# Optimization experiments

Measured on AMD Instinct MI355X. Metric: run time of the kernel, lower is better.

The kernel has to match this reference:

```python
import jax, jax.numpy as jnp
import numpy as np

D_MODEL = 1024
NUM_HEADS = 16
D_HEAD = D_MODEL // NUM_HEADS
ROPE_THETA = 10000.0


def _rope(x, pos):
    # x: [..., S, d_head]; rotate consecutive pairs (2i, 2i+1)
    half = x.shape[-1] // 2
    inv_freq = ROPE_THETA ** (-jnp.arange(half, dtype=jnp.float32) * 2.0 / x.shape[-1])
    ang = pos[:, None].astype(jnp.float32) * inv_freq[None, :]  # [S, half]
    cos, sin = jnp.cos(ang), jnp.sin(ang)
    x1, x2 = x[..., 0::2], x[..., 1::2]
    r1 = x1 * cos - x2 * sin
    r2 = x1 * sin + x2 * cos
    return jnp.stack([r1, r2], axis=-1).reshape(x.shape)


def setup_inputs() -> dict:
    key = jax.random.key(0)
    ks = jax.random.split(key, 5)
    s = 1.0 / np.sqrt(D_MODEL)
    return {
        "q_weight": jax.random.normal(ks[0], (D_MODEL, D_MODEL), jnp.float32) * s,
        "k_weight": jax.random.normal(ks[1], (D_MODEL, D_MODEL), jnp.float32) * s,
        "v_weight": jax.random.normal(ks[2], (D_MODEL, D_MODEL), jnp.float32) * s,
        "o_weight": jax.random.normal(ks[3], (D_MODEL, D_MODEL), jnp.float32) * s,
        "in_features": jax.random.normal(ks[4], (2, 2048, D_MODEL), jnp.float32),
    }


def reference(q_weight, k_weight, v_weight, o_weight, in_features):
    S = in_features.shape[-2]
    qw = q_weight.reshape(NUM_HEADS, D_HEAD, D_MODEL)
    kw = k_weight.reshape(NUM_HEADS, D_HEAD, D_MODEL)
    vw = v_weight.reshape(NUM_HEADS, D_HEAD, D_MODEL)
    # [B, H, S, d_head]
    q = jnp.einsum('bsj,nhj->bnsh', in_features, qw)
    k = jnp.einsum('bsj,nhj->bnsh', in_features, kw)
    v = jnp.einsum('bsj,nhj->bnsh', in_features, vw)
    pos = jnp.arange(S)
    q = _rope(q, pos)
    k = _rope(k, pos)
    scale = 1.0 / jnp.sqrt(jnp.asarray(D_HEAD, dtype=q.dtype))
    scores = jnp.einsum('bnqh,bnkh->bnqk', q, k) * scale  # [B,H,S,S]
    causal = jnp.tril(jnp.ones((S, S), dtype=bool))
    scores = jnp.where(causal, scores, jnp.asarray(-jnp.inf, dtype=scores.dtype))
    attn = jax.nn.softmax(scores, axis=-1)
    out = jnp.einsum('bnqk,bnkh->bnqh', attn, v)  # [B,H,S,d_head]
    out = jnp.swapaxes(out, -2, -3).reshape(*out.shape[:-3], S, D_MODEL)
    return jnp.einsum('ji,bki->bkj', o_weight, out)
```

## Files before the change

kernel.cpp:

```cpp
#include <hip/hip_runtime.h>
#include <math.h>

typedef __attribute__((ext_vector_type(8))) short bf16x8;
typedef __attribute__((ext_vector_type(4))) float f32x4;
typedef __attribute__((ext_vector_type(2))) unsigned int u32x2;

static constexpr int D_MODEL = 1024;
static constexpr int SEQ = 2048;
static constexpr int BATCH = 2;
static constexpr int M_TOT = BATCH * SEQ;

__device__ __forceinline__ unsigned short f2bf(float f) {
  unsigned int u = __builtin_bit_cast(unsigned int, f);
  u += 0x7fffu + ((u >> 16) & 1u);
  return (unsigned short)(u >> 16);
}

__device__ __forceinline__ unsigned int cvtpk(float lo, float hi) {
  unsigned int r;
  asm volatile("v_cvt_pk_bf16_f32 %0, %1, %2" : "=v"(r) : "v"(lo), "v"(hi));
  return r;
}

__device__ __forceinline__ void gld16(const unsigned short* g, unsigned short* l) {
  __builtin_amdgcn_global_load_lds(
      (const __attribute__((address_space(1))) unsigned int*)g,
      (__attribute__((address_space(3))) unsigned int*)l, 16, 0, 0);
}

__global__ void cvt_f32_bf16(const float* __restrict__ src,
                             unsigned short* __restrict__ dst, int n4) {
  int i = blockIdx.x * blockDim.x + threadIdx.x;
  if (i >= n4) return;
  const float4 v = reinterpret_cast<const float4*>(src)[i];
  ushort4 o;
  o.x = f2bf(v.x); o.y = f2bf(v.y); o.z = f2bf(v.z); o.w = f2bf(v.w);
  reinterpret_cast<ushort4*>(dst)[i] = o;
}

__global__ void cvt_weights(const float* __restrict__ qw, const float* __restrict__ kw,
                            const float* __restrict__ vw, const float* __restrict__ ow,
                            unsigned short* __restrict__ dst) {
  int i = blockIdx.x * blockDim.x + threadIdx.x;
  const int which = i >> 18;
  const int off = i & 262143;
  const float* src = (which == 0) ? qw : (which == 1) ? kw : (which == 2) ? vw : ow;
  const float4 v = reinterpret_cast<const float4*>(src)[off];
  ushort4 o;
  o.x = f2bf(v.x); o.y = f2bf(v.y); o.z = f2bf(v.z); o.w = f2bf(v.w);
  reinterpret_cast<ushort4*>(dst)[i] = o;
}

__global__ void rope_tables(float2* __restrict__ ct2) {
  int idx = blockIdx.x * blockDim.x + threadIdx.x;
  int s = idx >> 5;
  int p = idx & 31;
  float inv_freq = powf(10000.0f, -(float)p / 32.0f);
  float ang = (float)s * inv_freq;
  int psw = p ^ (((s >> 2) & 1) << 3);
  float2 cs; cs.x = cosf(ang); cs.y = sinf(ang);
  ct2[s * 32 + psw] = cs;
}

template <int BM, int BN, int MODE>
__global__ __launch_bounds__(256, 2)
void gemm2(const unsigned short* __restrict__ A,
           const unsigned short* __restrict__ W,
           unsigned short* __restrict__ Qd,
           unsigned short* __restrict__ Kd,
           unsigned short* __restrict__ Vd,
           float* __restrict__ Fd,
           const float2* __restrict__ ct2) {
  constexpr int MI = BM / 32, NI = BN / 32;
  constexpr int NKT = D_MODEL / 32;
  constexpr int LOADS = BM / 64 + BN / 64;
  __shared__ __align__(16) unsigned short smem[2 * (BM + BN) * 32];
  unsigned short* Asm = smem;
  unsigned short* Bsm = smem + 2 * BM * 32;
  const int tid  = threadIdx.x;
  const int lane = tid & 63;
  const int wave = tid >> 6;
  const int wm = wave >> 1, wn = wave & 1;
  const int m0 = blockIdx.y * BM;
  const int n0 = blockIdx.x * BN;
  const int lr = lane & 15, lg = lane >> 4;

  const int srow = lane >> 2;
  const int scol = ((lane & 3) ^ ((lane >> 3) & 3)) * 8;

  auto stage = [&](int buf, int kt) {
    const int k0 = kt * 32;
#pragma unroll
    for (int rr = 0; rr < BM / 64; ++rr) {
      const int ch = rr * 4 + wave;
      gld16(&A[(size_t)(m0 + ch * 16 + srow) * D_MODEL + k0 + scol], &Asm[buf * BM * 32 + ch * 512]);
    }
#pragma unroll
    for (int rr = 0; rr < BN / 64; ++rr) {
      const int ch = rr * 4 + wave;
      gld16(&W[(size_t)(n0 + ch * 16 + srow) * D_MODEL + k0 + scol], &Bsm[buf * BN * 32 + ch * 512]);
    }
  };

  f32x4 acc[MI][NI] = {};

  stage(0, 0);
  stage(1, 1);
  __builtin_amdgcn_sched_barrier(0);

  const int swz = (lg ^ ((lr >> 1) & 3)) * 8;

  for (int kt = 0; kt < NKT; ++kt) {
    const int cur = kt & 1;
    if (kt + 1 < NKT) {
      if constexpr (LOADS == 4) asm volatile("s_waitcnt vmcnt(4)" ::: "memory");
      else                      asm volatile("s_waitcnt vmcnt(3)" ::: "memory");
    } else {
      asm volatile("s_waitcnt vmcnt(0)" ::: "memory");
    }
    __builtin_amdgcn_s_barrier();
    __builtin_amdgcn_sched_barrier(0);

    bf16x8 af[MI], bfr[NI];
#pragma unroll
    for (int i = 0; i < MI; ++i)
      af[i] = *reinterpret_cast<const bf16x8*>(&Asm[cur * BM * 32 + (wm * (BM / 2) + i * 16 + lr) * 32 + swz]);
#pragma unroll
    for (int j = 0; j < NI; ++j)
      bfr[j] = *reinterpret_cast<const bf16x8*>(&Bsm[cur * BN * 32 + (wn * (BN / 2) + j * 16 + lr) * 32 + swz]);
    asm volatile("s_waitcnt lgkmcnt(0)" ::: "memory");
    __builtin_amdgcn_sched_barrier(0);
    __builtin_amdgcn_s_barrier();
    __builtin_amdgcn_sched_barrier(0);

    if (kt + 2 < NKT) stage(cur, kt + 2);
    __builtin_amdgcn_sched_barrier(0);

#pragma unroll
    for (int i = 0; i < MI; ++i)
#pragma unroll
      for (int j = 0; j < NI; ++j)
        acc[i][j] = __builtin_amdgcn_mfma_f32_16x16x32_bf16(af[i], bfr[j], acc[i][j], 0, 0, 0);
  }

  if constexpr (MODE == 2) {
#pragma unroll
    for (int i = 0; i < MI; ++i)
#pragma unroll
      for (int j = 0; j < NI; ++j)
#pragma unroll
        for (int r = 0; r < 4; ++r) {
          const int gm = m0 + wm * (BM / 2) + i * 16 + lg * 4 + r;
          const int gc = n0 + wn * (BN / 2) + j * 16 + lr;
          Fd[(size_t)gm * D_MODEL + gc] = acc[i][j][r];
        }
  } else {
    const int t = n0 >> 10;
    const int b = m0 >> 11;
    const int s_base = m0 & 2047;
    if (t < 2) {
      unsigned short* dstQ = (t == 0) ? Qd : Kd;
      const unsigned short* gsrc = (const unsigned short*)(ct2 + (size_t)s_base * 32);
#pragma unroll
      for (int it = 0; it < 8; ++it) {
        const int ch = wave * 8 + it;
        gld16(&gsrc[ch * 512 + lane * 8], &smem[ch * 512]);
      }
      asm volatile("s_waitcnt vmcnt(0)" ::: "memory");
      __builtin_amdgcn_sched_barrier(0);
      __builtin_amdgcn_s_barrier();
      const float2* tbl = (const float2*)smem;
      const int nbase = (n0 & 1023) >> 6;
#pragma unroll
      for (int i = 0; i < MI; ++i) {
#pragma unroll
        for (int j = 0; j < NI; ++j) {
#pragma unroll
          for (int r = 0; r < 4; ++r) {
            const int sl = wm * (BM / 2) + i * 16 + lg * 4 + r;
            const int h  = j * 16 + lr;
            const int psw = (h >> 1) ^ (((sl >> 2) & 1) << 3);
            const float2 cs = tbl[sl * 32 + psw];
            float x = acc[i][j][r];
            const float part = __shfl_xor(x, 1, 64);
            x = (h & 1) ? (part * cs.y + x * cs.x) : (x * cs.x - part * cs.y);
            const int n = nbase + wn;
            dstQ[(size_t)((b * 16 + n) * SEQ + s_base + sl) * 64 + h] = f2bf(x);
          }
        }
      }
    } else {
      unsigned short* tile = smem;
      const int row = tid >> 2;
      const int ck  = tid & 3;
      for (int pass = 0; pass < 2; ++pass) {
        __builtin_amdgcn_s_barrier();
        if (wn == pass) {
#pragma unroll
          for (int i = 0; i < MI; ++i)
#pragma unroll
            for (int j = 0; j < NI; ++j)
#pragma unroll
              for (int r = 0; r < 4; ++r)
                tile[(j * 16 + lr) * 136 + wm * 64 + i * 16 + lg * 4 + r] = f2bf(acc[i][j][r]);
        }
        asm volatile("s_waitcnt lgkmcnt(0)" ::: "memory");
        __builtin_amdgcn_sched_barrier(0);
        __builtin_amdgcn_s_barrier();
        const int c = (n0 & 1023) + pass * 64 + row;
        const int n = c >> 6, h = c & 63;
        unsigned short* vrow = &Vd[(size_t)((b * 16 + n) * 64 + h) * SEQ + s_base + ck * 32];
        const unsigned short* lrow = &tile[row * 136 + ck * 32];
#pragma unroll
        for (int k = 0; k < 4; ++k)
          *reinterpret_cast<bf16x8*>(&vrow[k * 8]) = *reinterpret_cast<const bf16x8*>(&lrow[k * 8]);
      }
    }
  }
}

__global__ __launch_bounds__(256, 2)
void attn_kernel(const unsigned short* __restrict__ Q,
                 const unsigned short* __restrict__ K,
                 const unsigned short* __restrict__ Vt,
                 unsigned short* __restrict__ AO) {
  __shared__ __align__(16) unsigned short Ksh[2][4096];
  __shared__ __align__(16) unsigned short Vsh[2][4096];
  __shared__ __align__(16) unsigned short Pl[4][32 * 72];
  const int bn   = blockIdx.x;
  const int j    = (gridDim.y - 1) - blockIdx.y;
  const int wave = threadIdx.x >> 6;
  const int lane = threadIdx.x & 63;
  const int lr = lane & 15, lg = lane >> 4;
  const int q0 = j * 128 + wave * 32;
  const unsigned short* Qh = Q  + (size_t)bn * SEQ * 64;
  const unsigned short* Kh = K  + (size_t)bn * SEQ * 64;
  const unsigned short* Vh = Vt + (size_t)bn * 64 * SEQ;
  unsigned short* Pw = &Pl[wave][0];
  const int b = bn >> 4, n = bn & 15;

  const int srow8 = lane >> 3;
  const int scolb = ((lane & 7) ^ srow8) * 8;

  auto stage = [&](int buf, int k0) {
#pragma unroll
    for (int c = 0; c < 2; ++c) {
      const int ch = wave * 2 + c;
      const int row = ch * 8 + srow8;
      gld16(&Kh[(size_t)(k0 + row) * 64 + scolb], &Ksh[buf][ch * 512]);
      gld16(&Vh[(size_t)row * SEQ + k0 + scolb], &Vsh[buf][ch * 512]);
    }
  };

  constexpr float KL2E = 0.125f * 1.44269504088896f;
  const int nt = 2 * j + 2;

  bf16x8 qf[2][2];
#pragma unroll
  for (int mi = 0; mi < 2; ++mi)
#pragma unroll
    for (int ks = 0; ks < 2; ++ks)
      qf[mi][ks] = *reinterpret_cast<const bf16x8*>(
          &Qh[(size_t)(q0 + mi * 16 + lr) * 64 + ks * 32 + lg * 8]);
  asm volatile("s_waitcnt vmcnt(0)" ::: "memory");
  __builtin_amdgcn_sched_barrier(0);

  f32x4 o[2][4] = {};
  float ls[2] = {0.f, 0.f};

  stage(0, 0);
  stage(1, 64);
  __builtin_amdgcn_sched_barrier(0);

  for (int t = 0; t < nt; ++t) {
    const int cur = t & 1;
    const int k0 = t * 64;
    if (t + 1 < nt) { asm volatile("s_waitcnt vmcnt(4)" ::: "memory"); }
    else            { asm volatile("s_waitcnt vmcnt(0)" ::: "memory"); }
    __builtin_amdgcn_s_barrier();
    __builtin_amdgcn_sched_barrier(0);

    const unsigned short* Kc = &Ksh[cur][0];
    const unsigned short* Vc = &Vsh[cur][0];

    bf16x8 kf[4][2];
#pragma unroll
    for (int nj = 0; nj < 4; ++nj)
#pragma unroll
      for (int ks = 0; ks < 2; ++ks) {
        const int R = nj * 16 + lr;
        const int p = (ks * 4 + lg) ^ (R & 7);
        kf[nj][ks] = *reinterpret_cast<const bf16x8*>(&Kc[R * 64 + p * 8]);
      }
    f32x4 sf[2][4] = {};
    __builtin_amdgcn_s_setprio(1);
#pragma unroll
    for (int nj = 0; nj < 4; ++nj)
#pragma unroll
      for (int ks = 0; ks < 2; ++ks)
#pragma unroll
        for (int mi = 0; mi < 2; ++mi)
          sf[mi][nj] = __builtin_amdgcn_mfma_f32_16x16x32_bf16(kf[nj][ks], qf[mi][ks], sf[mi][nj], 0, 0, 0);
    __builtin_amdgcn_s_setprio(0);

    bf16x8 vf[2][4];
#pragma unroll
    for (int ks2 = 0; ks2 < 2; ++ks2)
#pragma unroll
      for (int hf = 0; hf < 4; ++hf) {
        const int R = hf * 16 + lr;
        const int p = (ks2 * 4 + lg) ^ (R & 7);
        vf[ks2][hf] = *reinterpret_cast<const bf16x8*>(&Vc[R * 64 + p * 8]);
      }

    if (k0 + 63 <= q0) {
#pragma unroll
      for (int mi = 0; mi < 2; ++mi)
#pragma unroll
        for (int nj = 0; nj < 4; ++nj) {
          const float p0 = __builtin_amdgcn_exp2f(sf[mi][nj][0] * KL2E);
          const float p1 = __builtin_amdgcn_exp2f(sf[mi][nj][1] * KL2E);
          const float p2 = __builtin_amdgcn_exp2f(sf[mi][nj][2] * KL2E);
          const float p3 = __builtin_amdgcn_exp2f(sf[mi][nj][3] * KL2E);
          ls[mi] += (p0 + p1) + (p2 + p3);
          u32x2 w; w[0] = cvtpk(p0, p1); w[1] = cvtpk(p2, p3);
          *reinterpret_cast<u32x2*>(&Pw[(mi * 16 + lr) * 72 + nj * 16 + lg * 4]) = w;
        }
    } else {
#pragma unroll
      for (int mi = 0; mi < 2; ++mi) {
        const int qrow = q0 + mi * 16 + lr;
#pragma unroll
        for (int nj = 0; nj < 4; ++nj) {
          const int kb = k0 + nj * 16 + lg * 4;
          float p[4];
#pragma unroll
          for (int r = 0; r < 4; ++r)
            p[r] = (kb + r <= qrow) ? __builtin_amdgcn_exp2f(sf[mi][nj][r] * KL2E) : 0.0f;
          ls[mi] += (p[0] + p[1]) + (p[2] + p[3]);
          u32x2 w; w[0] = cvtpk(p[0], p[1]); w[1] = cvtpk(p[2], p[3]);
          *reinterpret_cast<u32x2*>(&Pw[(mi * 16 + lr) * 72 + nj * 16 + lg * 4]) = w;
        }
      }
    }

    asm volatile("s_waitcnt lgkmcnt(0)" ::: "memory");
    __builtin_amdgcn_sched_barrier(0);
    __builtin_amdgcn_s_barrier();
    __builtin_amdgcn_sched_barrier(0);

    if (t + 2 < nt) stage(cur, (t + 2) * 64);
    __builtin_amdgcn_sched_barrier(0);

    bf16x8 pf[2][2];
#pragma unroll
    for (int mi = 0; mi < 2; ++mi)
#pragma unroll
      for (int ks2 = 0; ks2 < 2; ++ks2)
        pf[mi][ks2] = *reinterpret_cast<const bf16x8*>(&Pw[(mi * 16 + lr) * 72 + ks2 * 32 + lg * 8]);
    __builtin_amdgcn_s_setprio(1);
#pragma unroll
    for (int ks2 = 0; ks2 < 2; ++ks2)
#pragma unroll
      for (int hf = 0; hf < 4; ++hf)
#pragma unroll
        for (int mi = 0; mi < 2; ++mi)
          o[mi][hf] = __builtin_amdgcn_mfma_f32_16x16x32_bf16(pf[mi][ks2], vf[ks2][hf], o[mi][hf], 0, 0, 0);
    __builtin_amdgcn_s_setprio(0);
  }

#pragma unroll
  for (int mi = 0; mi < 2; ++mi) {
    float s = ls[mi];
    s += __shfl_xor(s, 16, 64);
    s += __shfl_xor(s, 32, 64);
    ls[mi] = s;
  }
#pragma unroll
  for (int mi = 0; mi < 2; ++mi)
#pragma unroll
    for (int r = 0; r < 4; ++r) {
      const float sv = __shfl(ls[mi], lg * 4 + r, 64);
      const float inv = 1.0f / sv;
      const int srow = q0 + mi * 16 + lg * 4 + r;
#pragma unroll
      for (int hf = 0; hf < 4; ++hf) {
        const int h = hf * 16 + lr;
        AO[(size_t)(b * SEQ + srow) * D_MODEL + n * 64 + h] = f2bf(o[mi][hf][r] * inv);
      }
    }
}

extern "C" void kernel_launch(void* const* d_in, const int* in_sizes, int n_in,
                              void* d_out, int out_size, void* d_ws, size_t ws_size,
                              hipStream_t stream) {
  const float* qw = (const float*)d_in[0];
  const float* kw = (const float*)d_in[1];
  const float* vw = (const float*)d_in[2];
  const float* ow = (const float*)d_in[3];
  const float* x  = (const float*)d_in[4];

  char* ws = (char*)d_ws;
  const size_t XB = (size_t)M_TOT * D_MODEL * 2;
  const size_t WB = (size_t)D_MODEL * D_MODEL * 2;
  unsigned short* Xb  = (unsigned short*)ws;  ws += XB;
  unsigned short* Wqb = (unsigned short*)ws;  ws += WB;
  unsigned short* Wkb = (unsigned short*)ws;  ws += WB;
  unsigned short* Wvb = (unsigned short*)ws;  ws += WB;
  unsigned short* Wob = (unsigned short*)ws;  ws += WB;
  unsigned short* Qr  = (unsigned short*)ws;  ws += XB;
  unsigned short* Kr  = (unsigned short*)ws;  ws += XB;
  unsigned short* Vt  = (unsigned short*)ws;  ws += XB;
  unsigned short* AO  = (unsigned short*)ws;  ws += XB;
  float2* ct2 = (float2*)ws;  ws += (size_t)SEQ * 32 * 8;
  (void)Wkb; (void)Wvb;

  cvt_f32_bf16<<<(M_TOT * D_MODEL / 4) / 256, 256, 0, stream>>>(x, Xb, M_TOT * D_MODEL / 4);
  cvt_weights<<<(4 * D_MODEL * D_MODEL / 4) / 256, 256, 0, stream>>>(qw, kw, vw, ow, Wqb);
  rope_tables<<<(SEQ * 32) / 256, 256, 0, stream>>>(ct2);

  gemm2<128, 128, 0><<<dim3(3072 / 128, M_TOT / 128), 256, 0, stream>>>(
      Xb, Wqb, Qr, Kr, Vt, nullptr, ct2);

  attn_kernel<<<dim3(BATCH * 16, 16), 256, 0, stream>>>(Qr, Kr, Vt, AO);

  gemm2<128, 64, 2><<<dim3(D_MODEL / 64, M_TOT / 128), 256, 0, stream>>>(
      AO, Wob, nullptr, nullptr, nullptr, (float*)d_out, nullptr);
}
```

Before: 105.6 us.

## Triple-buffer GEMM and attention LDS staging to drop a barrier per iteration

Both the projection GEMM and the attention kernel move from two to three LDS buffers. Each iteration now issues the prefetch for tile t+2 into the third buffer right after the first barrier, which removes the second workgroup barrier per iteration. The attention P scratch also gets an XOR swizzle on its writes and reads to cut LDS bank conflicts. The cost is more LDS per block, which may limit two-blocks-per-CU occupancy, especially for the larger GEMM tiles. An extra barrier is added before the GEMM epilogue reuses smem.

```diff
diff --git a/kernel.cpp b/kernel.cpp
--- a/kernel.cpp
+++ b/kernel.cpp
@@ -74,9 +74,9 @@
   constexpr int MI = BM / 32, NI = BN / 32;
   constexpr int NKT = D_MODEL / 32;
   constexpr int LOADS = BM / 64 + BN / 64;
-  __shared__ __align__(16) unsigned short smem[2 * (BM + BN) * 32];
+  __shared__ __align__(16) unsigned short smem[3 * (BM + BN) * 32];
   unsigned short* Asm = smem;
-  unsigned short* Bsm = smem + 2 * BM * 32;
+  unsigned short* Bsm = smem + 3 * BM * 32;
   const int tid  = threadIdx.x;
   const int lane = tid & 63;
   const int wave = tid >> 6;
@@ -110,8 +110,8 @@
 
   const int swz = (lg ^ ((lr >> 1) & 3)) * 8;
 
+  int cur = 0;
   for (int kt = 0; kt < NKT; ++kt) {
-    const int cur = kt & 1;
     if (kt + 1 < NKT) {
       if constexpr (LOADS == 4) asm volatile("s_waitcnt vmcnt(4)" ::: "memory");
       else                      asm volatile("s_waitcnt vmcnt(3)" ::: "memory");
@@ -121,6 +121,12 @@
     __builtin_amdgcn_s_barrier();
     __builtin_amdgcn_sched_barrier(0);
 
+    if (kt + 2 < NKT) {
+      int nb = cur + 2; if (nb >= 3) nb -= 3;
+      stage(nb, kt + 2);
+    }
+    __builtin_amdgcn_sched_barrier(0);
+
     bf16x8 af[MI], bfr[NI];
 #pragma unroll
     for (int i = 0; i < MI; ++i)
@@ -130,17 +136,14 @@
       bfr[j] = *reinterpret_cast<const bf16x8*>(&Bsm[cur * BN * 32 + (wn * (BN / 2) + j * 16 + lr) * 32 + swz]);
     asm volatile("s_waitcnt lgkmcnt(0)" ::: "memory");
     __builtin_amdgcn_sched_barrier(0);
-    __builtin_amdgcn_s_barrier();
-    __builtin_amdgcn_sched_barrier(0);
-
-    if (kt + 2 < NKT) stage(cur, kt + 2);
-    __builtin_amdgcn_sched_barrier(0);
 
 #pragma unroll
     for (int i = 0; i < MI; ++i)
 #pragma unroll
       for (int j = 0; j < NI; ++j)
         acc[i][j] = __builtin_amdgcn_mfma_f32_16x16x32_bf16(af[i], bfr[j], acc[i][j], 0, 0, 0);
+
+    cur = (cur == 2) ? 0 : cur + 1;
   }
 
   if constexpr (MODE == 2) {
@@ -155,6 +158,7 @@
           Fd[(size_t)gm * D_MODEL + gc] = acc[i][j][r];
         }
   } else {
+    __builtin_amdgcn_s_barrier();
     const int t = n0 >> 10;
     const int b = m0 >> 11;
     const int s_base = m0 & 2047;
@@ -224,8 +228,8 @@
                  const unsigned short* __restrict__ K,
                  const unsigned short* __restrict__ Vt,
                  unsigned short* __restrict__ AO) {
-  __shared__ __align__(16) unsigned short Ksh[2][4096];
-  __shared__ __align__(16) unsigned short Vsh[2][4096];
+  __shared__ __align__(16) unsigned short Ksh[3 * 4096];
+  __shared__ __align__(16) unsigned short Vsh[3 * 4096];
   __shared__ __align__(16) unsigned short Pl[4][32 * 72];
   const int bn   = blockIdx.x;
   const int j    = (gridDim.y - 1) - blockIdx.y;
@@ -247,8 +251,8 @@
     for (int c = 0; c < 2; ++c) {
       const int ch = wave * 2 + c;
       const int row = ch * 8 + srow8;
-      gld16(&Kh[(size_t)(k0 + row) * 64 + scolb], &Ksh[buf][ch * 512]);
-      gld16(&Vh[(size_t)row * SEQ + k0 + scolb], &Vsh[buf][ch * 512]);
+      gld16(&Kh[(size_t)(k0 + row) * 64 + scolb], &Ksh[buf * 4096 + ch * 512]);
+      gld16(&Vh[(size_t)row * SEQ + k0 + scolb], &Vsh[buf * 4096 + ch * 512]);
     }
   };
 
@@ -272,16 +276,22 @@
   stage(1, 64);
   __builtin_amdgcn_sched_barrier(0);
 
+  int cur = 0;
   for (int t = 0; t < nt; ++t) {
-    const int cur = t & 1;
     const int k0 = t * 64;
     if (t + 1 < nt) { asm volatile("s_waitcnt vmcnt(4)" ::: "memory"); }
     else            { asm volatile("s_waitcnt vmcnt(0)" ::: "memory"); }
     __builtin_amdgcn_s_barrier();
     __builtin_amdgcn_sched_barrier(0);
 
-    const unsigned short* Kc = &Ksh[cur][0];
-    const unsigned short* Vc = &Vsh[cur][0];
+    if (t + 2 < nt) {
+      int nb = cur + 2; if (nb >= 3) nb -= 3;
+      stage(nb, (t + 2) * 64);
+    }
+    __builtin_amdgcn_sched_barrier(0);
+
+    const unsigned short* Kc = &Ksh[cur * 4096];
+    const unsigned short* Vc = &Vsh[cur * 4096];
 
     bf16x8 kf[4][2];
 #pragma unroll
@@ -324,7 +334,8 @@
           const float p3 = __builtin_amdgcn_exp2f(sf[mi][nj][3] * KL2E);
           ls[mi] += (p0 + p1) + (p2 + p3);
           u32x2 w; w[0] = cvtpk(p0, p1); w[1] = cvtpk(p2, p3);
-          *reinterpret_cast<u32x2*>(&Pw[(mi * 16 + lr) * 72 + nj * 16 + lg * 4]) = w;
+          const int cw = ((nj * 4 + lg) ^ ((lr & 3) << 1)) * 4;
+          *reinterpret_cast<u32x2*>(&Pw[(mi * 16 + lr) * 72 + cw]) = w;
         }
     } else {
 #pragma unroll
@@ -339,25 +350,23 @@
             p[r] = (kb + r <= qrow) ? __builtin_amdgcn_exp2f(sf[mi][nj][r] * KL2E) : 0.0f;
           ls[mi] += (p[0] + p[1]) + (p[2] + p[3]);
           u32x2 w; w[0] = cvtpk(p[0], p[1]); w[1] = cvtpk(p[2], p[3]);
-          *reinterpret_cast<u32x2*>(&Pw[(mi * 16 + lr) * 72 + nj * 16 + lg * 4]) = w;
+          const int cw = ((nj * 4 + lg) ^ ((lr & 3) << 1)) * 4;
+          *reinterpret_cast<u32x2*>(&Pw[(mi * 16 + lr) * 72 + cw]) = w;
         }
       }
     }
 
     asm volatile("s_waitcnt lgkmcnt(0)" ::: "memory");
     __builtin_amdgcn_sched_barrier(0);
-    __builtin_amdgcn_s_barrier();
-    __builtin_amdgcn_sched_barrier(0);
-
-    if (t + 2 < nt) stage(cur, (t + 2) * 64);
-    __builtin_amdgcn_sched_barrier(0);
 
     bf16x8 pf[2][2];
 #pragma unroll
     for (int mi = 0; mi < 2; ++mi)
 #pragma unroll
-      for (int ks2 = 0; ks2 < 2; ++ks2)
-        pf[mi][ks2] = *reinterpret_cast<const bf16x8*>(&Pw[(mi * 16 + lr) * 72 + ks2 * 32 + lg * 8]);
+      for (int ks2 = 0; ks2 < 2; ++ks2) {
+        const int cr = ((ks2 * 4 + lg) ^ (lr & 3)) * 8;
+        pf[mi][ks2] = *reinterpret_cast<const bf16x8*>(&Pw[(mi * 16 + lr) * 72 + cr]);
+      }
     __builtin_amdgcn_s_setprio(1);
 #pragma unroll
     for (int ks2 = 0; ks2 < 2; ++ks2)
@@ -367,6 +376,8 @@
         for (int mi = 0; mi < 2; ++mi)
           o[mi][hf] = __builtin_amdgcn_mfma_f32_16x16x32_bf16(pf[mi][ks2], vf[ks2][hf], o[mi][hf], 0, 0, 0);
     __builtin_amdgcn_s_setprio(0);
+
+    cur = (cur == 2) ? 0 : cur + 1;
   }
 
 #pragma unroll
```

Measured after the change: 115.4 us. +9.3%, slower.

## Keep softmax probabilities in registers and use 16x16x16 MFMA for PV

Applied to the files above, without the earlier changes.

Drops the per-wave LDS round trip for the probability tile. The packed bf16 P values now stay in registers and feed the PV product directly through the 16x16x16 bf16 MFMA, whose A-operand layout matches the QK^T accumulator layout. V fragments are reloaded from LDS as 4-element chunks to fit the new k-split. This removes the LDS writes and reads of P and frees shared memory, but it doubles the MFMA instruction count for PV using a lower-throughput instruction shape and adds more, smaller V loads.

```diff
diff --git a/kernel.cpp b/kernel.cpp
--- a/kernel.cpp
+++ b/kernel.cpp
@@ -2,6 +2,7 @@
 #include <math.h>
 
 typedef __attribute__((ext_vector_type(8))) short bf16x8;
+typedef __attribute__((ext_vector_type(4))) short bf16x4;
 typedef __attribute__((ext_vector_type(4))) float f32x4;
 typedef __attribute__((ext_vector_type(2))) unsigned int u32x2;
 
@@ -226,7 +227,6 @@
                  unsigned short* __restrict__ AO) {
   __shared__ __align__(16) unsigned short Ksh[2][4096];
   __shared__ __align__(16) unsigned short Vsh[2][4096];
-  __shared__ __align__(16) unsigned short Pl[4][32 * 72];
   const int bn   = blockIdx.x;
   const int j    = (gridDim.y - 1) - blockIdx.y;
   const int wave = threadIdx.x >> 6;
@@ -236,7 +236,6 @@
   const unsigned short* Qh = Q  + (size_t)bn * SEQ * 64;
   const unsigned short* Kh = K  + (size_t)bn * SEQ * 64;
   const unsigned short* Vh = Vt + (size_t)bn * 64 * SEQ;
-  unsigned short* Pw = &Pl[wave][0];
   const int b = bn >> 4, n = bn & 15;
 
   const int srow8 = lane >> 3;
@@ -303,16 +302,18 @@
           sf[mi][nj] = __builtin_amdgcn_mfma_f32_16x16x32_bf16(kf[nj][ks], qf[mi][ks], sf[mi][nj], 0, 0, 0);
     __builtin_amdgcn_s_setprio(0);
 
-    bf16x8 vf[2][4];
-#pragma unroll
-    for (int ks2 = 0; ks2 < 2; ++ks2)
+    bf16x4 vB[4][4];
+#pragma unroll
+    for (int nj = 0; nj < 4; ++nj)
 #pragma unroll
       for (int hf = 0; hf < 4; ++hf) {
         const int R = hf * 16 + lr;
-        const int p = (ks2 * 4 + lg) ^ (R & 7);
-        vf[ks2][hf] = *reinterpret_cast<const bf16x8*>(&Vc[R * 64 + p * 8]);
-      }
-
+        const int c = nj * 2 + (lg >> 1);
+        const int p = ((c ^ (R & 7)) << 3) + (lg & 1) * 4;
+        vB[nj][hf] = *reinterpret_cast<const bf16x4*>(&Vc[R * 64 + p]);
+      }
+
+    u32x2 w[2][4];
     if (k0 + 63 <= q0) {
 #pragma unroll
       for (int mi = 0; mi < 2; ++mi)
@@ -323,8 +324,8 @@
           const float p2 = __builtin_amdgcn_exp2f(sf[mi][nj][2] * KL2E);
           const float p3 = __builtin_amdgcn_exp2f(sf[mi][nj][3] * KL2E);
           ls[mi] += (p0 + p1) + (p2 + p3);
-          u32x2 w; w[0] = cvtpk(p0, p1); w[1] = cvtpk(p2, p3);
-          *reinterpret_cast<u32x2*>(&Pw[(mi * 16 + lr) * 72 + nj * 16 + lg * 4]) = w;
+          w[mi][nj][0] = cvtpk(p0, p1);
+          w[mi][nj][1] = cvtpk(p2, p3);
         }
     } else {
 #pragma unroll
@@ -338,8 +339,8 @@
           for (int r = 0; r < 4; ++r)
             p[r] = (kb + r <= qrow) ? __builtin_amdgcn_exp2f(sf[mi][nj][r] * KL2E) : 0.0f;
           ls[mi] += (p[0] + p[1]) + (p[2] + p[3]);
-          u32x2 w; w[0] = cvtpk(p[0], p[1]); w[1] = cvtpk(p[2], p[3]);
-          *reinterpret_cast<u32x2*>(&Pw[(mi * 16 + lr) * 72 + nj * 16 + lg * 4]) = w;
+          w[mi][nj][0] = cvtpk(p[0], p[1]);
+          w[mi][nj][1] = cvtpk(p[2], p[3]);
         }
       }
     }
@@ -352,20 +353,15 @@
     if (t + 2 < nt) stage(cur, (t + 2) * 64);
     __builtin_amdgcn_sched_barrier(0);
 
-    bf16x8 pf[2][2];
-#pragma unroll
-    for (int mi = 0; mi < 2; ++mi)
-#pragma unroll
-      for (int ks2 = 0; ks2 < 2; ++ks2)
-        pf[mi][ks2] = *reinterpret_cast<const bf16x8*>(&Pw[(mi * 16 + lr) * 72 + ks2 * 32 + lg * 8]);
     __builtin_amdgcn_s_setprio(1);
 #pragma unroll
-    for (int ks2 = 0; ks2 < 2; ++ks2)
+    for (int nj = 0; nj < 4; ++nj)
 #pragma unroll
       for (int hf = 0; hf < 4; ++hf)
 #pragma unroll
         for (int mi = 0; mi < 2; ++mi)
-          o[mi][hf] = __builtin_amdgcn_mfma_f32_16x16x32_bf16(pf[mi][ks2], vf[ks2][hf], o[mi][hf], 0, 0, 0);
+          o[mi][hf] = __builtin_amdgcn_mfma_f32_16x16x16bf16_1k(
+              __builtin_bit_cast(bf16x4, w[mi][nj]), vB[nj][hf], o[mi][hf], 0, 0, 0);
     __builtin_amdgcn_s_setprio(0);
   }
 
```

Measured after the change: 105.5 us. About the same (-0.1%).
